# Optimization experiments

Measured on AMD Instinct MI355X. Metric: run time of the kernel, lower is better.

The kernel has to match this reference:

```python
import jax, jax.numpy as jnp
import numpy as np
import math

HID = 2048
NH = 8
KVH = 1
HD = 256
REP = NH // KVH
THETA = 10000.0
B, S = 2, 2048
NEG = -1e9  # additive mask value for disallowed positions


def setup_inputs() -> dict:
    key = jax.random.key(0)
    ks = jax.random.split(key, 6)
    x = jax.random.normal(ks[0], (B, S, HID), dtype=jnp.float32)
    # causal additive mask [B,1,S,S]
    causal = jnp.tril(jnp.ones((S, S), dtype=bool))
    attn_mask = jnp.where(causal, 0.0, NEG).astype(jnp.float32)[None, None]
    attn_mask = jnp.broadcast_to(attn_mask, (B, 1, S, S))
    pos_ids = jnp.broadcast_to(jnp.arange(S, dtype=jnp.int64 if jax.config.jax_enable_x64 else jnp.int32), (B, S))
    sc = 0.02
    wq = jax.random.normal(ks[1], (HID, NH * HD), dtype=jnp.float32) * sc
    wk = jax.random.normal(ks[2], (HID, KVH * HD), dtype=jnp.float32) * sc
    wv = jax.random.normal(ks[3], (HID, KVH * HD), dtype=jnp.float32) * sc
    wo = jax.random.normal(ks[4], (NH * HD, HID), dtype=jnp.float32) * sc
    return {"x": x, "attn_mask": attn_mask, "pos_ids": pos_ids,
            "wq": wq, "wk": wk, "wv": wv, "wo": wo}


def _rotate_half(t):
    h = t.shape[-1] // 2
    return jnp.concatenate([-t[..., h:], t[..., :h]], axis=-1)


def _rope_cos_sin(pos_ids, dtype):
    inv_freq = 1.0 / (THETA ** (jnp.arange(0, HD, 2, dtype=jnp.float32) / HD))  # [HD/2]
    freqs = pos_ids.astype(jnp.float32)[:, :, None] * inv_freq[None, None, :]  # [B,S,HD/2]
    emb = jnp.concatenate([freqs, freqs], axis=-1)                              # [B,S,HD]
    # unsqueeze head dim -> [B,1,S,HD]
    return jnp.cos(emb)[:, None].astype(dtype), jnp.sin(emb)[:, None].astype(dtype)


def reference(x, attn_mask, pos_ids, wq, wk, wv, wo):
    b, s, _ = x.shape
    q = (x @ wq).reshape(b, s, NH, HD).transpose(0, 2, 1, 3)    # [B,NH,S,HD]
    k = (x @ wk).reshape(b, s, KVH, HD).transpose(0, 2, 1, 3)   # [B,KVH,S,HD]
    v = (x @ wv).reshape(b, s, KVH, HD).transpose(0, 2, 1, 3)   # [B,KVH,S,HD]
    cos, sin = _rope_cos_sin(pos_ids, q.dtype)
    q = q * cos + _rotate_half(q) * sin
    k = k * cos + _rotate_half(k) * sin
    # GQA: group query heads over shared KV head instead of materializing repeat_kv
    qg = q.reshape(b, KVH, REP, s, HD)
    scores = jnp.einsum('bgrqd,bgkd->bgrqk', qg, k) / math.sqrt(HD)  # [B,KVH,REP,S,S]
    scores = scores.reshape(b, NH, s, s) + attn_mask
    attn = jax.nn.softmax(scores.astype(jnp.float32), axis=-1).astype(q.dtype)  # [B,NH,S,S]
    # dropout p=0.0 -> identity
    pg = attn.reshape(b, KVH, REP, s, s)
    out = jnp.einsum('bgrqk,bgkd->bgrqd', pg, v).reshape(b, NH, s, HD)
    out = out.transpose(0, 2, 1, 3).reshape(b, s, NH * HD) @ wo  # [B,S,HID]
    return out, attn
```

## Files before the change

### kernel.cpp

```cpp
#include <hip/hip_runtime.h>
#include <cstdint>
#include <cmath>

#define HID_ 2048
#define NH_ 8
#define HD_ 256
#define B_ 2
#define S_ 2048
#define BS_ (B_*S_)
#define QKVW_ 2560

typedef short short8 __attribute__((ext_vector_type(8)));
typedef float floatx4 __attribute__((ext_vector_type(4)));

static __device__ __forceinline__ unsigned short f2bf(float f) {
  union { float f; unsigned u; } v; v.f = f;
  return (unsigned short)((v.u + 0x7FFFu + ((v.u >> 16) & 1u)) >> 16);
}
static __device__ __forceinline__ float bf2f(unsigned short h) {
  union { unsigned u; float f; } v; v.u = ((unsigned)h) << 16;
  return v.f;
}

static __device__ __forceinline__ void gload_lds16(const void* g, void* l) {
  __builtin_amdgcn_global_load_lds(
      (const __attribute__((address_space(1))) unsigned int*)g,
      (__attribute__((address_space(3))) unsigned int*)l, 16, 0, 0);
}


__global__ void cast_f32_bf16_k(const float* __restrict__ in, unsigned short* __restrict__ out, long n) {
  long i = ((long)blockIdx.x * blockDim.x + threadIdx.x) * 4;
  if (i >= n) return;
  float4 v = *reinterpret_cast<const float4*>(in + i);
  ushort4 o; o.x = f2bf(v.x); o.y = f2bf(v.y); o.z = f2bf(v.z); o.w = f2bf(v.w);
  *reinterpret_cast<ushort4*>(out + i) = o;
}

__global__ void transpose_f2b_k(const float* __restrict__ in, unsigned short* __restrict__ out, int R, int C) {
  __shared__ float tile[32][33];
  int c0 = blockIdx.x * 32, r0 = blockIdx.y * 32;
  int tx = threadIdx.x, ty = threadIdx.y;
  #pragma unroll
  for (int i = 0; i < 4; i++)
    tile[ty + i*8][tx] = in[(long)(r0 + ty + i*8) * C + c0 + tx];
  __syncthreads();
  #pragma unroll
  for (int i = 0; i < 4; i++)
    out[(long)(c0 + ty + i*8) * R + r0 + tx] = f2bf(tile[tx][ty + i*8]);
}

__global__ void transpose_strided_k(const unsigned short* __restrict__ in, unsigned short* __restrict__ out,
                                    int ld_in, int ld_out, long in_bs, long out_bs) {
  __shared__ unsigned short tile[32][33];
  in += (long)blockIdx.z * in_bs; out += (long)blockIdx.z * out_bs;
  int c0 = blockIdx.x * 32, r0 = blockIdx.y * 32;
  int tx = threadIdx.x, ty = threadIdx.y;
  #pragma unroll
  for (int i = 0; i < 4; i++)
    tile[ty + i*8][tx] = in[(long)(r0 + ty + i*8) * ld_in + c0 + tx];
  __syncthreads();
  #pragma unroll
  for (int i = 0; i < 4; i++)
    out[(long)(c0 + ty + i*8) * ld_out + r0 + tx] = tile[tx][ty + i*8];
}

__global__ void rope_k(unsigned short* __restrict__ qk, const int* __restrict__ pos_ids,
                       int heads, int row_stride, long total) {
  long idx = (long)blockIdx.x * blockDim.x + threadIdx.x;
  if (idx >= total) return;
  int per_row = heads * (HD_/2);
  int r  = (int)(idx / per_row);
  int rem = (int)(idx % per_row);
  int h = rem / (HD_/2);
  int i = rem % (HD_/2);
  float posf = (float)pos_ids[r];
  float freq = expf(-(float)i * (logf(10000.0f) / 128.0f));
  float ang = posf * freq;
  float c = cosf(ang), s = sinf(ang);
  unsigned short* p = qk + (long)r * row_stride + (long)h * HD_;
  float a = bf2f(p[i]), b = bf2f(p[i + 128]);
  p[i]       = f2bf(a * c - b * s);
  p[i + 128] = f2bf(b * c + a * s);
}

template<int EPI>
__global__ __launch_bounds__(256)
void gemm_bt_k(const void* __restrict__ Av, const unsigned short* __restrict__ Bt,
               void* __restrict__ Cv, int K, long lda, long ldb, long ldc, int inner_div,
               long a_so, long a_si, long b_so, long b_si, long c_so, long c_si,
               float scale, float* __restrict__ partials) {
  int z = blockIdx.z;
  int zo = z / inner_div, zi = z % inner_div;
  long a_off = (long)zo * a_so + (long)zi * a_si;
  long b_off = (long)zo * b_so + (long)zi * b_si;
  long c_off = (long)zo * c_so + (long)zi * c_si;

  __shared__ unsigned short Al[128 * 32];
  __shared__ unsigned short Bl[128 * 32];
  __shared__ float sumsp[128][2];

  int tid = threadIdx.x;
  int lane = tid & 63, wave = tid >> 6;
  int bm = blockIdx.y * 128, bn = blockIdx.x * 128;

  const unsigned short* Abase = (const unsigned short*)Av + a_off + (long)bm * lda;
  const unsigned short* Bbase = Bt + b_off + (long)bn * ldb;

  floatx4 zero = {0.f, 0.f, 0.f, 0.f};
  floatx4 acc[4][4];
  #pragma unroll
  for (int i = 0; i < 4; i++)
    #pragma unroll
    for (int j = 0; j < 4; j++) acc[i][j] = zero;

  int kend = K;
  if (EPI == 2) { if (bn > bm + 127) kend = 0; }

  const int wm = (wave >> 1) * 64, wn = (wave & 1) * 64;
  const int lr = lane & 15, lq = lane >> 4;

  for (int k0 = 0; k0 < kend; k0 += 32) {
    #pragma unroll
    for (int c = 0; c < 2; c++) {
      int e = c * 2048 + tid * 8;
      int row = e >> 5, col = e & 31;
      gload_lds16(Abase + (long)row * lda + k0 + col, (char*)Al + c * 4096 + wave * 1024);
    }
    #pragma unroll
    for (int c = 0; c < 2; c++) {
      int e = c * 2048 + tid * 8;
      int row = e >> 5, col = e & 31;
      gload_lds16(Bbase + (long)row * ldb + k0 + col, (char*)Bl + c * 4096 + wave * 1024);
    }
    __syncthreads();

    short8 af[4], bfr[4];
    #pragma unroll
    for (int i = 0; i < 4; i++)
      af[i] = *reinterpret_cast<const short8*>(&Al[(wm + i*16 + lr) * 32 + lq * 8]);
    #pragma unroll
    for (int j = 0; j < 4; j++)
      bfr[j] = *reinterpret_cast<const short8*>(&Bl[(wn + j*16 + lr) * 32 + lq * 8]);
    #pragma unroll
    for (int i = 0; i < 4; i++)
      #pragma unroll
      for (int j = 0; j < 4; j++)
        acc[i][j] = __builtin_amdgcn_mfma_f32_16x16x32_bf16(af[i], bfr[j], acc[i][j], 0, 0, 0);
    __syncthreads();
  }

  if (EPI == 0) {
    unsigned short* C = (unsigned short*)Cv + c_off;
    #pragma unroll
    for (int i = 0; i < 4; i++)
      #pragma unroll
      for (int r = 0; r < 4; r++) {
        int row = bm + wm + i*16 + lq*4 + r;
        #pragma unroll
        for (int j = 0; j < 4; j++) {
          int col = bn + wn + j*16 + lr;
          C[(long)row * ldc + col] = f2bf(acc[i][j][r] * scale);
        }
      }
  } else if (EPI == 1) {
    float* C = (float*)Cv + c_off;
    #pragma unroll
    for (int i = 0; i < 4; i++)
      #pragma unroll
      for (int r = 0; r < 4; r++) {
        int row = bm + wm + i*16 + lq*4 + r;
        #pragma unroll
        for (int j = 0; j < 4; j++) {
          int col = bn + wn + j*16 + lr;
          C[(long)row * ldc + col] = acc[i][j][r] * scale;
        }
      }
  } else {
    float* C = (float*)Cv + c_off;
    #pragma unroll
    for (int i = 0; i < 4; i++)
      #pragma unroll
      for (int r = 0; r < 4; r++) {
        int rl = wm + i*16 + lq*4 + r;
        int row = bm + rl;
        float s_ir = 0.f;
        #pragma unroll
        for (int j = 0; j < 4; j++) {
          int col = bn + wn + j*16 + lr;
          float pv = (col <= row) ? __expf(acc[i][j][r] * scale) : 0.0f;
          C[(long)row * ldc + col] = pv;
          s_ir += pv;
        }
        #pragma unroll
        for (int o = 1; o < 16; o <<= 1) s_ir += __shfl_xor(s_ir, o, 64);
        if (lr == 0) sumsp[rl][wave & 1] = s_ir;
      }
    __syncthreads();
    if (tid < 128)
      partials[((long)z * S_ + bm + tid) * 16 + blockIdx.x] = sumsp[tid][0] + sumsp[tid][1];
  }
}

__global__ __launch_bounds__(256)
void pv_k(float* __restrict__ attn, const unsigned short* __restrict__ v_t,
          const float* __restrict__ partials, unsigned short* __restrict__ o_bf) {
  int z = blockIdx.y;
  int b = z >> 3, h = z & 7;
  int bm = blockIdx.x * 64;
  float* A = attn + (long)z * S_ * S_;
  const unsigned short* Bv = v_t + (long)b * HD_ * S_;
  unsigned short* C = o_bf + (long)b * S_ * HID_ + h * HD_;

  __shared__ unsigned short Al[64 * 32];
  __shared__ unsigned short Bl[256 * 32];
  __shared__ float inv[64];

  int tid = threadIdx.x;
  int lane = tid & 63, wave = tid >> 6;
  int lr = lane & 15, lq = lane >> 4;

  if (tid < 64) {
    const float* pp = partials + ((long)z * S_ + bm + tid) * 16;
    float s = 0.f;
    #pragma unroll
    for (int t = 0; t < 16; t++) s += pp[t];
    inv[tid] = 1.0f / s;
  }
  __syncthreads();

  floatx4 zero = {0.f, 0.f, 0.f, 0.f};
  floatx4 acc[16];
  #pragma unroll
  for (int j = 0; j < 16; j++) acc[j] = zero;

  int kend = bm + 64;
  for (int k0 = 0; k0 < kend; k0 += 32) {
    {
      int e = tid * 8;
      int row = e >> 5, col = e & 31;
      long g = (long)(bm + row) * S_ + k0 + col;
      float4 v0 = *reinterpret_cast<const float4*>(&A[g]);
      float4 v1 = *reinterpret_cast<const float4*>(&A[g + 4]);
      float iv = inv[row];
      v0.x *= iv; v0.y *= iv; v0.z *= iv; v0.w *= iv;
      v1.x *= iv; v1.y *= iv; v1.z *= iv; v1.w *= iv;
      *reinterpret_cast<float4*>(&A[g])     = v0;
      *reinterpret_cast<float4*>(&A[g + 4]) = v1;
      short8 o8;
      o8[0]=(short)f2bf(v0.x); o8[1]=(short)f2bf(v0.y); o8[2]=(short)f2bf(v0.z); o8[3]=(short)f2bf(v0.w);
      o8[4]=(short)f2bf(v1.x); o8[5]=(short)f2bf(v1.y); o8[6]=(short)f2bf(v1.z); o8[7]=(short)f2bf(v1.w);
      *reinterpret_cast<short8*>(&Al[e]) = o8;
    }
    #pragma unroll
    for (int c = 0; c < 4; c++) {
      int e = c * 2048 + tid * 8;
      int row = e >> 5, col = e & 31;
      gload_lds16(Bv + (long)row * S_ + k0 + col, (char*)Bl + c * 4096 + wave * 1024);
    }
    __syncthreads();

    short8 af = *reinterpret_cast<const short8*>(&Al[(wave*16 + lr) * 32 + lq * 8]);
    #pragma unroll
    for (int j = 0; j < 16; j++) {
      short8 bfr = *reinterpret_cast<const short8*>(&Bl[(j*16 + lr) * 32 + lq * 8]);
      acc[j] = __builtin_amdgcn_mfma_f32_16x16x32_bf16(af, bfr, acc[j], 0, 0, 0);
    }
    __syncthreads();
  }

  #pragma unroll
  for (int j = 0; j < 16; j++)
    #pragma unroll
    for (int r = 0; r < 4; r++) {
      int row = bm + wave*16 + lq*4 + r;
      int col = j*16 + lr;
      C[(long)row * HID_ + col] = f2bf(acc[j][r]);
    }
}


extern "C" void kernel_launch(void* const* d_in, const int* in_sizes, int n_in,
                              void* d_out, int out_size, void* d_ws, size_t ws_size,
                              hipStream_t stream) {
  (void)in_sizes; (void)n_in; (void)out_size; (void)ws_size;
  const float* x   = (const float*)d_in[0];
  const int*   pos = (const int*)d_in[2];
  const float* wq  = (const float*)d_in[3];
  const float* wk  = (const float*)d_in[4];
  const float* wv  = (const float*)d_in[5];
  const float* wo  = (const float*)d_in[6];
  float* out  = (float*)d_out;
  float* attn = out + (long)B_ * S_ * HID_;

  char* p = (char*)d_ws;
  auto take = [&](size_t n) { char* r = p; p += (n + 255) & ~(size_t)255; return r; };
  unsigned short* x_bf   = (unsigned short*)take((size_t)BS_ * HID_ * 2);
  unsigned short* wqkv_t = (unsigned short*)take((size_t)QKVW_ * HID_ * 2);
  unsigned short* wo_t   = (unsigned short*)take((size_t)HID_ * HID_ * 2);
  unsigned short* qkv    = (unsigned short*)take((size_t)BS_ * QKVW_ * 2);
  unsigned short* v_t    = (unsigned short*)take((size_t)B_ * HD_ * S_ * 2);
  unsigned short* o_bf   = (unsigned short*)take((size_t)BS_ * HID_ * 2);
  float*          parts  = (float*)take((size_t)B_ * NH_ * S_ * 16 * 4);

  dim3 tb(32, 8);

  cast_f32_bf16_k<<<(BS_ * HID_) / 1024, 256, 0, stream>>>(x, x_bf, (long)BS_ * HID_);

  transpose_f2b_k<<<dim3(HID_/32, HID_/32), tb, 0, stream>>>(wq, wqkv_t, HID_, HID_);
  transpose_f2b_k<<<dim3(HD_/32,  HID_/32), tb, 0, stream>>>(wk, wqkv_t + (size_t)2048 * HID_, HID_, HD_);
  transpose_f2b_k<<<dim3(HD_/32,  HID_/32), tb, 0, stream>>>(wv, wqkv_t + (size_t)2304 * HID_, HID_, HD_);
  transpose_f2b_k<<<dim3(HID_/32, HID_/32), tb, 0, stream>>>(wo, wo_t, HID_, HID_);

  gemm_bt_k<0><<<dim3(QKVW_/128, BS_/128, 1), 256, 0, stream>>>(
      x_bf, wqkv_t, qkv, HID_, HID_, HID_, QKVW_, 1, 0,0,0,0,0,0, 1.0f, nullptr);

  rope_k<<<(BS_ * NH_ * (HD_/2)) / 256, 256, 0, stream>>>(
      qkv, pos, NH_, QKVW_, (long)BS_ * NH_ * (HD_/2));
  rope_k<<<(BS_ * (HD_/2)) / 256, 256, 0, stream>>>(
      qkv + 2048, pos, 1, QKVW_, (long)BS_ * (HD_/2));

  transpose_strided_k<<<dim3(HD_/32, S_/32, B_), tb, 0, stream>>>(
      qkv + 2304, v_t, QKVW_, S_, (long)S_ * QKVW_, (long)HD_ * S_);

  gemm_bt_k<2><<<dim3(S_/128, S_/128, B_ * NH_), 256, 0, stream>>>(
      qkv, qkv + 2048, attn, HD_, QKVW_, QKVW_, S_, NH_,
      (long)S_ * QKVW_, (long)HD_, (long)S_ * QKVW_, 0,
      (long)NH_ * S_ * S_, (long)S_ * S_, 0.0625f, parts);

  pv_k<<<dim3(S_/64, B_ * NH_), 256, 0, stream>>>(attn, v_t, parts, o_bf);

  gemm_bt_k<1><<<dim3(HID_/128, BS_/128, 1), 256, 0, stream>>>(
      o_bf, wo_t, out, HID_, HID_, HID_, HID_, 1, 0,0,0,0,0,0, 1.0f, nullptr);
}
```

Measured before the change: 697.8 us.

## Fuse QK^T, softmax and PV into one two-pass attention kernel

```diff
diff --git a/kernel.cpp b/kernel.cpp
--- a/kernel.cpp
+++ b/kernel.cpp
@@ -87,25 +87,16 @@
 template<int EPI>
 __global__ __launch_bounds__(256)
 void gemm_bt_k(const void* __restrict__ Av, const unsigned short* __restrict__ Bt,
-               void* __restrict__ Cv, int K, long lda, long ldb, long ldc, int inner_div,
-               long a_so, long a_si, long b_so, long b_si, long c_so, long c_si,
-               float scale, float* __restrict__ partials) {
-  int z = blockIdx.z;
-  int zo = z / inner_div, zi = z % inner_div;
-  long a_off = (long)zo * a_so + (long)zi * a_si;
-  long b_off = (long)zo * b_so + (long)zi * b_si;
-  long c_off = (long)zo * c_so + (long)zi * c_si;
-
+               void* __restrict__ Cv, int K, long lda, long ldb, long ldc) {
   __shared__ unsigned short Al[128 * 32];
   __shared__ unsigned short Bl[128 * 32];
-  __shared__ float sumsp[128][2];
 
   int tid = threadIdx.x;
   int lane = tid & 63, wave = tid >> 6;
   int bm = blockIdx.y * 128, bn = blockIdx.x * 128;
 
-  const unsigned short* Abase = (const unsigned short*)Av + a_off + (long)bm * lda;
-  const unsigned short* Bbase = Bt + b_off + (long)bn * ldb;
+  const unsigned short* Abase = (const unsigned short*)Av + (long)bm * lda;
+  const unsigned short* Bbase = Bt + (long)bn * ldb;
 
   floatx4 zero = {0.f, 0.f, 0.f, 0.f};
   floatx4 acc[4][4];
@@ -114,13 +105,10 @@
     #pragma unroll
     for (int j = 0; j < 4; j++) acc[i][j] = zero;
 
-  int kend = K;
-  if (EPI == 2) { if (bn > bm + 127) kend = 0; }
-
   const int wm = (wave >> 1) * 64, wn = (wave & 1) * 64;
   const int lr = lane & 15, lq = lane >> 4;
 
-  for (int k0 = 0; k0 < kend; k0 += 32) {
+  for (int k0 = 0; k0 < K; k0 += 32) {
     #pragma unroll
     for (int c = 0; c < 2; c++) {
       int e = c * 2048 + tid * 8;
@@ -151,7 +139,7 @@
   }
 
   if (EPI == 0) {
-    unsigned short* C = (unsigned short*)Cv + c_off;
+    unsigned short* C = (unsigned short*)Cv;
     #pragma unroll
     for (int i = 0; i < 4; i++)
       #pragma unroll
@@ -160,11 +148,11 @@
         #pragma unroll
         for (int j = 0; j < 4; j++) {
           int col = bn + wn + j*16 + lr;
-          C[(long)row * ldc + col] = f2bf(acc[i][j][r] * scale);
+          C[(long)row * ldc + col] = f2bf(acc[i][j][r]);
         }
       }
-  } else if (EPI == 1) {
-    float* C = (float*)Cv + c_off;
+  } else {
+    float* C = (float*)Cv;
     #pragma unroll
     for (int i = 0; i < 4; i++)
       #pragma unroll
@@ -173,109 +161,161 @@
         #pragma unroll
         for (int j = 0; j < 4; j++) {
           int col = bn + wn + j*16 + lr;
-          C[(long)row * ldc + col] = acc[i][j][r] * scale;
+          C[(long)row * ldc + col] = acc[i][j][r];
         }
       }
-  } else {
-    float* C = (float*)Cv + c_off;
-    #pragma unroll
-    for (int i = 0; i < 4; i++)
-      #pragma unroll
-      for (int r = 0; r < 4; r++) {
-        int rl = wm + i*16 + lq*4 + r;
-        int row = bm + rl;
-        float s_ir = 0.f;
-        #pragma unroll
-        for (int j = 0; j < 4; j++) {
-          int col = bn + wn + j*16 + lr;
-          float pv = (col <= row) ? __expf(acc[i][j][r] * scale) : 0.0f;
-          C[(long)row * ldc + col] = pv;
-          s_ir += pv;
-        }
-        #pragma unroll
-        for (int o = 1; o < 16; o <<= 1) s_ir += __shfl_xor(s_ir, o, 64);
-        if (lr == 0) sumsp[rl][wave & 1] = s_ir;
-      }
-    __syncthreads();
-    if (tid < 128)
-      partials[((long)z * S_ + bm + tid) * 16 + blockIdx.x] = sumsp[tid][0] + sumsp[tid][1];
-  }
-}
-
-__global__ __launch_bounds__(256)
-void pv_k(float* __restrict__ attn, const unsigned short* __restrict__ v_t,
-          const float* __restrict__ partials, unsigned short* __restrict__ o_bf) {
-  int z = blockIdx.y;
+  }
+}
+
+__global__ __launch_bounds__(256, 2)
+void attn_fused_k(const unsigned short* __restrict__ qkv, const unsigned short* __restrict__ v_t,
+                  float* __restrict__ attn, unsigned short* __restrict__ o_bf) {
+  int z = blockIdx.x;
   int b = z >> 3, h = z & 7;
-  int bm = blockIdx.x * 64;
-  float* A = attn + (long)z * S_ * S_;
-  const unsigned short* Bv = v_t + (long)b * HD_ * S_;
-  unsigned short* C = o_bf + (long)b * S_ * HID_ + h * HD_;
-
-  __shared__ unsigned short Al[64 * 32];
-  __shared__ unsigned short Bl[256 * 32];
-  __shared__ float inv[64];
+  int t = 31 - blockIdx.y;
+  int bm = t * 64;
+  int nkt = t / 2 + 1;
+
+  const unsigned short* Qg = qkv + (long)b * S_ * QKVW_ + (long)h * HD_;
+  const unsigned short* Kg = qkv + (long)b * S_ * QKVW_ + 2048;
+  const unsigned short* Vt = v_t + (long)b * HD_ * S_;
+  float* Az = attn + (long)z * S_ * S_;
+
+  __shared__ unsigned short Ql[64 * 256];
+  __shared__ unsigned short Kl[128 * 32];
+  __shared__ unsigned short Pl[64 * 128];
+  __shared__ unsigned short Vl[256 * 32];
+  __shared__ float ssum[64];
 
   int tid = threadIdx.x;
   int lane = tid & 63, wave = tid >> 6;
   int lr = lane & 15, lq = lane >> 4;
 
-  if (tid < 64) {
-    const float* pp = partials + ((long)z * S_ + bm + tid) * 16;
-    float s = 0.f;
-    #pragma unroll
-    for (int t = 0; t < 16; t++) s += pp[t];
-    inv[tid] = 1.0f / s;
+  {
+    int ce = nkt * 128;
+    int perrow = (S_ - ce) >> 2;
+    float4 zf = {0.f, 0.f, 0.f, 0.f};
+    for (int i = tid; i < 64 * perrow; i += 256) {
+      int r = i / perrow, c = i - r * perrow;
+      *reinterpret_cast<float4*>(Az + (long)(bm + r) * S_ + ce + c * 4) = zf;
+    }
+  }
+
+  #pragma unroll
+  for (int c = 0; c < 8; c++) {
+    int idx = c * 2048 + tid * 8;
+    int row = idx >> 8, col = idx & 255;
+    gload_lds16(Qg + (long)(bm + row) * QKVW_ + col, (char*)Ql + c * 4096 + wave * 1024);
+  }
+
+  floatx4 zero = {0.f, 0.f, 0.f, 0.f};
+
+  float rsum[4] = {0.f, 0.f, 0.f, 0.f};
+  for (int kt = 0; kt < nkt; kt++) {
+    floatx4 sacc[8];
+    #pragma unroll
+    for (int j = 0; j < 8; j++) sacc[j] = zero;
+    for (int k0 = 0; k0 < HD_; k0 += 32) {
+      #pragma unroll
+      for (int c = 0; c < 2; c++) {
+        int e = c * 2048 + tid * 8;
+        int row = e >> 5, col = e & 31;
+        gload_lds16(Kg + (long)(kt * 128 + row) * QKVW_ + k0 + col, (char*)Kl + c * 4096 + wave * 1024);
+      }
+      __syncthreads();
+      short8 aq = *reinterpret_cast<const short8*>(&Ql[(wave*16 + lr) * 256 + k0 + lq * 8]);
+      #pragma unroll
+      for (int j = 0; j < 8; j++) {
+        short8 bk = *reinterpret_cast<const short8*>(&Kl[(j*16 + lr) * 32 + lq * 8]);
+        sacc[j] = __builtin_amdgcn_mfma_f32_16x16x32_bf16(aq, bk, sacc[j], 0, 0, 0);
+      }
+      __syncthreads();
+    }
+    #pragma unroll
+    for (int j = 0; j < 8; j++)
+      #pragma unroll
+      for (int r = 0; r < 4; r++) {
+        int row_l = wave*16 + lq*4 + r;
+        int col_g = kt*128 + j*16 + lr;
+        float p = (col_g <= bm + row_l) ? __expf(sacc[j][r] * 0.0625f) : 0.f;
+        rsum[r] += p;
+      }
+  }
+  #pragma unroll
+  for (int r = 0; r < 4; r++) {
+    float s = rsum[r];
+    #pragma unroll
+    for (int o = 1; o < 16; o <<= 1) s += __shfl_xor(s, o, 64);
+    if (lr == 0) ssum[wave*16 + lq*4 + r] = s;
   }
   __syncthreads();
 
-  floatx4 zero = {0.f, 0.f, 0.f, 0.f};
-  floatx4 acc[16];
-  #pragma unroll
-  for (int j = 0; j < 16; j++) acc[j] = zero;
-
-  int kend = bm + 64;
-  for (int k0 = 0; k0 < kend; k0 += 32) {
-    {
-      int e = tid * 8;
-      int row = e >> 5, col = e & 31;
-      long g = (long)(bm + row) * S_ + k0 + col;
-      float4 v0 = *reinterpret_cast<const float4*>(&A[g]);
-      float4 v1 = *reinterpret_cast<const float4*>(&A[g + 4]);
-      float iv = inv[row];
-      v0.x *= iv; v0.y *= iv; v0.z *= iv; v0.w *= iv;
-      v1.x *= iv; v1.y *= iv; v1.z *= iv; v1.w *= iv;
-      *reinterpret_cast<float4*>(&A[g])     = v0;
-      *reinterpret_cast<float4*>(&A[g + 4]) = v1;
-      short8 o8;
-      o8[0]=(short)f2bf(v0.x); o8[1]=(short)f2bf(v0.y); o8[2]=(short)f2bf(v0.z); o8[3]=(short)f2bf(v0.w);
-      o8[4]=(short)f2bf(v1.x); o8[5]=(short)f2bf(v1.y); o8[6]=(short)f2bf(v1.z); o8[7]=(short)f2bf(v1.w);
-      *reinterpret_cast<short8*>(&Al[e]) = o8;
-    }
-    #pragma unroll
-    for (int c = 0; c < 4; c++) {
-      int e = c * 2048 + tid * 8;
-      int row = e >> 5, col = e & 31;
-      gload_lds16(Bv + (long)row * S_ + k0 + col, (char*)Bl + c * 4096 + wave * 1024);
-    }
+  float inv[4];
+  #pragma unroll
+  for (int r = 0; r < 4; r++) inv[r] = 1.0f / ssum[wave*16 + lq*4 + r];
+
+  floatx4 oacc[16];
+  #pragma unroll
+  for (int j = 0; j < 16; j++) oacc[j] = zero;
+
+  for (int kt = 0; kt < nkt; kt++) {
+    floatx4 sacc[8];
+    #pragma unroll
+    for (int j = 0; j < 8; j++) sacc[j] = zero;
+    for (int k0 = 0; k0 < HD_; k0 += 32) {
+      #pragma unroll
+      for (int c = 0; c < 2; c++) {
+        int e = c * 2048 + tid * 8;
+        int row = e >> 5, col = e & 31;
+        gload_lds16(Kg + (long)(kt * 128 + row) * QKVW_ + k0 + col, (char*)Kl + c * 4096 + wave * 1024);
+      }
+      __syncthreads();
+      short8 aq = *reinterpret_cast<const short8*>(&Ql[(wave*16 + lr) * 256 + k0 + lq * 8]);
+      #pragma unroll
+      for (int j = 0; j < 8; j++) {
+        short8 bk = *reinterpret_cast<const short8*>(&Kl[(j*16 + lr) * 32 + lq * 8]);
+        sacc[j] = __builtin_amdgcn_mfma_f32_16x16x32_bf16(aq, bk, sacc[j], 0, 0, 0);
+      }
+      __syncthreads();
+    }
+    #pragma unroll
+    for (int j = 0; j < 8; j++)
+      #pragma unroll
+      for (int r = 0; r < 4; r++) {
+        int row_l = wave*16 + lq*4 + r;
+        int col_g = kt*128 + j*16 + lr;
+        float p = (col_g <= bm + row_l) ? __expf(sacc[j][r] * 0.0625f) * inv[r] : 0.f;
+        Az[(long)(bm + row_l) * S_ + col_g] = p;
+        Pl[row_l * 128 + j*16 + lr] = f2bf(p);
+      }
     __syncthreads();
-
-    short8 af = *reinterpret_cast<const short8*>(&Al[(wave*16 + lr) * 32 + lq * 8]);
-    #pragma unroll
-    for (int j = 0; j < 16; j++) {
-      short8 bfr = *reinterpret_cast<const short8*>(&Bl[(j*16 + lr) * 32 + lq * 8]);
-      acc[j] = __builtin_amdgcn_mfma_f32_16x16x32_bf16(af, bfr, acc[j], 0, 0, 0);
-    }
-    __syncthreads();
-  }
-
-  #pragma unroll
-  for (int j = 0; j < 16; j++)
+    #pragma unroll
+    for (int kk = 0; kk < 4; kk++) {
+      #pragma unroll
+      for (int c = 0; c < 4; c++) {
+        int e = c * 2048 + tid * 8;
+        int row = e >> 5, col = e & 31;
+        gload_lds16(Vt + (long)row * S_ + kt*128 + kk*32 + col, (char*)Vl + c * 4096 + wave * 1024);
+      }
+      __syncthreads();
+      short8 ap = *reinterpret_cast<const short8*>(&Pl[(wave*16 + lr) * 128 + kk*32 + lq * 8]);
+      #pragma unroll
+      for (int j2 = 0; j2 < 16; j2++) {
+        short8 bv = *reinterpret_cast<const short8*>(&Vl[(j2*16 + lr) * 32 + lq * 8]);
+        oacc[j2] = __builtin_amdgcn_mfma_f32_16x16x32_bf16(ap, bv, oacc[j2], 0, 0, 0);
+      }
+      __syncthreads();
+    }
+  }
+
+  unsigned short* C = o_bf + (long)b * S_ * HID_ + (long)h * HD_;
+  #pragma unroll
+  for (int j2 = 0; j2 < 16; j2++)
     #pragma unroll
     for (int r = 0; r < 4; r++) {
       int row = bm + wave*16 + lq*4 + r;
-      int col = j*16 + lr;
-      C[(long)row * HID_ + col] = f2bf(acc[j][r]);
+      int col = j2*16 + lr;
+      C[(long)row * HID_ + col] = f2bf(oacc[j2][r]);
     }
 }
 
@@ -301,7 +341,6 @@
   unsigned short* qkv    = (unsigned short*)take((size_t)BS_ * QKVW_ * 2);
   unsigned short* v_t    = (unsigned short*)take((size_t)B_ * HD_ * S_ * 2);
   unsigned short* o_bf   = (unsigned short*)take((size_t)BS_ * HID_ * 2);
-  float*          parts  = (float*)take((size_t)B_ * NH_ * S_ * 16 * 4);
 
   dim3 tb(32, 8);
 
@@ -312,8 +351,8 @@
   transpose_f2b_k<<<dim3(HD_/32,  HID_/32), tb, 0, stream>>>(wv, wqkv_t + (size_t)2304 * HID_, HID_, HD_);
   transpose_f2b_k<<<dim3(HID_/32, HID_/32), tb, 0, stream>>>(wo, wo_t, HID_, HID_);
 
-  gemm_bt_k<0><<<dim3(QKVW_/128, BS_/128, 1), 256, 0, stream>>>(
-      x_bf, wqkv_t, qkv, HID_, HID_, HID_, QKVW_, 1, 0,0,0,0,0,0, 1.0f, nullptr);
+  gemm_bt_k<0><<<dim3(QKVW_/128, BS_/128), 256, 0, stream>>>(
+      x_bf, wqkv_t, qkv, HID_, HID_, HID_, QKVW_);
 
   rope_k<<<(BS_ * NH_ * (HD_/2)) / 256, 256, 0, stream>>>(
       qkv, pos, NH_, QKVW_, (long)BS_ * NH_ * (HD_/2));
@@ -323,13 +362,8 @@
   transpose_strided_k<<<dim3(HD_/32, S_/32, B_), tb, 0, stream>>>(
       qkv + 2304, v_t, QKVW_, S_, (long)S_ * QKVW_, (long)HD_ * S_);
 
-  gemm_bt_k<2><<<dim3(S_/128, S_/128, B_ * NH_), 256, 0, stream>>>(
-      qkv, qkv + 2048, attn, HD_, QKVW_, QKVW_, S_, NH_,
-      (long)S_ * QKVW_, (long)HD_, (long)S_ * QKVW_, 0,
-      (long)NH_ * S_ * S_, (long)S_ * S_, 0.0625f, parts);
-
-  pv_k<<<dim3(S_/64, B_ * NH_), 256, 0, stream>>>(attn, v_t, parts, o_bf);
-
-  gemm_bt_k<1><<<dim3(HID_/128, BS_/128, 1), 256, 0, stream>>>(
-      o_bf, wo_t, out, HID_, HID_, HID_, HID_, 1, 0,0,0,0,0,0, 1.0f, nullptr);
-}
+  attn_fused_k<<<dim3(B_ * NH_, S_/64), 256, 0, stream>>>(qkv, v_t, attn, o_bf);
+
+  gemm_bt_k<1><<<dim3(HID_/128, BS_/128), 256, 0, stream>>>(
+      o_bf, wo_t, out, HID_, HID_, HID_, HID_);
+}
```

After: 661.4 us. -5.2%, faster.
